# Kernel optimization log

Measured on AMD Instinct MI355X. Metric: run time of the kernel, lower is better.

## Reference

```python
import jax, jax.numpy as jnp
import numpy as np

C = 512
GROUPS = 8
EPS = 1e-5


def setup_inputs() -> dict:
    key = jax.random.key(0)
    ks = jax.random.split(key, 7)
    B, H, W = 16, 32, 32
    x = jax.random.normal(ks[0], (B, C, H, W), dtype=jnp.float32)
    gamma = jnp.ones((C,), jnp.float32)
    beta = jnp.zeros((C,), jnp.float32)
    # 1x1 convs stored as [out, in] matrices
    w_qkv = jax.random.normal(ks[1], (3 * C, C), dtype=jnp.float32) * (1.0 / np.sqrt(C))
    b_qkv = jax.random.normal(ks[2], (3 * C,), dtype=jnp.float32) * 0.02
    w_proj = jax.random.normal(ks[3], (C, C), dtype=jnp.float32) * (1.0 / np.sqrt(C))
    b_proj = jax.random.normal(ks[4], (C,), dtype=jnp.float32) * 0.02
    return {"x": x, "gamma": gamma, "beta": beta, "w_qkv": w_qkv,
            "b_qkv": b_qkv, "w_proj": w_proj, "b_proj": b_proj}


def _group_norm(x, gamma, beta):
    B, Cc, H, W = x.shape
    xg = x.reshape(B, GROUPS, Cc // GROUPS, H, W)
    mean = xg.mean(axis=(2, 3, 4), keepdims=True)
    var = xg.var(axis=(2, 3, 4), keepdims=True)
    xg = (xg - mean) * jax.lax.rsqrt(var + EPS)
    x = xg.reshape(B, Cc, H, W)
    return x * gamma[None, :, None, None] + beta[None, :, None, None]


def reference(x, gamma, beta, w_qkv, b_qkv, w_proj, b_proj):
    B, Cc, H, W = x.shape
    N = H * W
    h = _group_norm(x, gamma, beta)  # [B,C,H,W]
    hf = h.reshape(B, Cc, N)  # [B,C,N]
    # 1x1 conv == matmul over channel dim
    qkv = jnp.einsum('oc,bcn->bon', w_qkv, hf) + b_qkv[None, :, None]  # [B,3C,N]
    q, k, v = jnp.split(qkv, 3, axis=1)  # each [B,C,N]
    scale = 1.0 / jnp.sqrt(jnp.float32(Cc))
    # attn[b,i,j] = sum_c q[b,c,i] * k[b,c,j]
    attn = jnp.einsum('bci,bcj->bij', q, k) * scale  # [B,N,N]
    attn = jax.nn.softmax(attn, axis=-1)
    out = jnp.einsum('bij,bcj->bci', attn, v)  # [B,C,N]
    out = jnp.einsum('oc,bcn->bon', w_proj, out) + b_proj[None, :, None]
    return x + out.reshape(B, Cc, H, W)
```

## Files before the change

kernel.cpp:

```cpp
#include <hip/hip_runtime.h>
#include <hip/hip_bf16.h>

typedef unsigned short u16;
typedef unsigned int u32;
typedef __attribute__((ext_vector_type(8))) short short8;
typedef __attribute__((ext_vector_type(4))) float floatx4;

#define BATCH 16
#define CDIM 512
#define NSPAT 1024
#define NGROUP 8

__device__ __forceinline__ u16 f2bf(float f) {
    unsigned u = __float_as_uint(f);
    u += 0x7FFFu + ((u >> 16) & 1u);
    return (u16)(u >> 16);
}
__device__ __forceinline__ u32 f2bf2(float lo, float hi) {
    __hip_bfloat162 h = __float22bfloat162_rn(make_float2(lo, hi));
    return *(u32*)&h;
}

__device__ __forceinline__ void load_lds16(const void* g, void* l) {
    __builtin_amdgcn_global_load_lds(
        (const __attribute__((address_space(1))) unsigned int*)g,
        (__attribute__((address_space(3))) unsigned int*)l, 16, 0, 0);
}

__global__ __launch_bounds__(256) void prep_kernel(
    const float* __restrict__ w_qkv, const float* __restrict__ w_proj,
    const float* __restrict__ b_qkv, const float* __restrict__ x,
    u16* __restrict__ wmega, u16* __restrict__ wproj_bf, u16* __restrict__ wv_t,
    float* __restrict__ stats, float* __restrict__ lsums, float* __restrict__ bpv) {
    int b = blockIdx.x;
    int tid = threadIdx.x;
    if (b < 768) {
        const float* src = (b < 512) ? w_qkv : w_proj;
        u16* dst = (b < 512) ? wmega : wproj_bf;
        int i = (b < 512 ? b : b - 512) * 256 + tid;
        float4 v = ((const float4*)src)[i];
        u32* d = (u32*)dst;
        d[i * 2] = f2bf2(v.x, v.y);
        d[i * 2 + 1] = f2bf2(v.z, v.w);
        return;
    }
    if (b < 832) {
        __shared__ u16 t[64 * 66];
        int bt = b - 768;
        int tx = bt & 7, ty = bt >> 3;
        const float* src = w_qkv + (size_t)(1024 + ty * 64) * CDIM + tx * 64;
#pragma unroll
        for (int p = 0; p < 4; ++p) {
            int r = p * 16 + (tid >> 4);
            int c4 = (tid & 15) << 2;
            float4 v = *(const float4*)(src + (size_t)r * CDIM + c4);
            u16* d = &t[r * 66 + c4];
            d[0] = f2bf(v.x); d[1] = f2bf(v.y); d[2] = f2bf(v.z); d[3] = f2bf(v.w);
        }
        __syncthreads();
        u16* dst = wv_t + (size_t)(tx * 64) * CDIM + ty * 64;
#pragma unroll
        for (int p = 0; p < 4; ++p) {
            int c = p * 16 + (tid >> 4);
            int r4 = (tid & 15) << 2;
            ushort4 o;
            o.x = t[(r4 + 0) * 66 + c];
            o.y = t[(r4 + 1) * 66 + c];
            o.z = t[(r4 + 2) * 66 + c];
            o.w = t[(r4 + 3) * 66 + c];
            *(ushort4*)(dst + (size_t)c * CDIM + r4) = o;
        }
        return;
    }
    if (b < 960) {
        __shared__ float rs[4], rss[4];
        int bg = b - 832;
        const float4* xv = (const float4*)(x + (size_t)bg * 65536);
        float s = 0.f, ss = 0.f;
        for (int i = tid; i < 16384; i += 256) {
            float4 v = xv[i];
            s += v.x + v.y + v.z + v.w;
            ss += v.x * v.x + v.y * v.y + v.z * v.z + v.w * v.w;
        }
#pragma unroll
        for (int off = 32; off; off >>= 1) { s += __shfl_down(s, off); ss += __shfl_down(ss, off); }
        int wave = tid >> 6, lane = tid & 63;
        if (lane == 0) { rs[wave] = s; rss[wave] = ss; }
        __syncthreads();
        if (tid == 0) {
            float S1 = rs[0] + rs[1] + rs[2] + rs[3];
            float S2 = rss[0] + rss[1] + rss[2] + rss[3];
            float mean = S1 * (1.f / 65536.f);
            float var = S2 * (1.f / 65536.f) - mean * mean;
            stats[bg * 2] = mean;
            stats[bg * 2 + 1] = rsqrtf(var + 1e-5f);
        }
        return;
    }
    if (b < 976) {
        ((float4*)lsums)[(b - 960) * 256 + tid] = (float4){0.f, 0.f, 0.f, 0.f};
        return;
    }
    {
        int o0 = (b - 976) * 64;
        int wave = tid >> 6, lane = tid & 63;
        const float4* bvv = (const float4*)(b_qkv + 1024);
        float4 v0 = bvv[lane * 2], v1 = bvv[lane * 2 + 1];
        for (int it = 0; it < 16; ++it) {
            int o = o0 + wave * 16 + it;
            const float4* wr = (const float4*)(w_proj + (size_t)o * CDIM);
            float4 a0 = wr[lane * 2], a1 = wr[lane * 2 + 1];
            float s = a0.x * v0.x + a0.y * v0.y + a0.z * v0.z + a0.w * v0.w
                    + a1.x * v1.x + a1.y * v1.y + a1.z * v1.z + a1.w * v1.w;
#pragma unroll
            for (int off = 32; off; off >>= 1) s += __shfl_down(s, off);
            if (lane == 0) bpv[o] = s;
        }
    }
}

__device__ __forceinline__ void gemm_core(
    const u16* __restrict__ Ab, const u16* __restrict__ Bb, int K, int lda, int ldb,
    int m0, int n0, u16* As, u16* Bs, floatx4 (&acc)[4][4]) {
    int tid = threadIdx.x;
    int lane = tid & 63, wave = tid >> 6, quad = lane >> 4, lrow = lane & 15;
    int wm = (wave >> 1) << 6, wn = (wave & 1) << 6;
    for (int k0 = 0; k0 < K; k0 += 64) {
#pragma unroll
        for (int it = 0; it < 4; ++it) {
            int c = it * 256 + tid;
            int r = c >> 3, p = c & 7;
            int kc = p ^ (r & 7);
            load_lds16(Ab + (size_t)(m0 + r) * lda + k0 + (kc << 3), &As[c << 3]);
            load_lds16(Bb + (size_t)(n0 + r) * ldb + k0 + (kc << 3), &Bs[c << 3]);
        }
        __syncthreads();
#pragma unroll
        for (int s = 0; s < 2; ++s) {
            short8 af[4], bf[4];
#pragma unroll
            for (int i = 0; i < 4; ++i) {
                int R = wm + i * 16 + lrow;
                int p = (s * 4 + quad) ^ (R & 7);
                af[i] = *(const short8*)&As[(R << 6) + (p << 3)];
            }
#pragma unroll
            for (int j = 0; j < 4; ++j) {
                int R = wn + j * 16 + lrow;
                int p = (s * 4 + quad) ^ (R & 7);
                bf[j] = *(const short8*)&Bs[(R << 6) + (p << 3)];
            }
#pragma unroll
            for (int i = 0; i < 4; ++i)
#pragma unroll
                for (int j = 0; j < 4; ++j)
                    acc[i][j] = __builtin_amdgcn_mfma_f32_16x16x32_bf16(af[i], bf[j], acc[i][j], 0, 0, 0);
        }
        __syncthreads();
    }
}

#define ACC_INIT floatx4 acc[4][4]; \
    _Pragma("unroll") for (int i = 0; i < 4; ++i) \
    _Pragma("unroll") for (int j = 0; j < 4; ++j) acc[i][j] = (floatx4){0.f, 0.f, 0.f, 0.f};

#define EPILOG_IDX int lane = threadIdx.x & 63, wave = threadIdx.x >> 6; \
    int quad = lane >> 4, lrow = lane & 15; \
    int wm = (wave >> 1) << 6, wn = (wave & 1) << 6;

#define TSTR 66
__global__ __launch_bounds__(256) void gn_wpv_kernel(
    const float* __restrict__ x, const float* __restrict__ gamma, const float* __restrict__ beta,
    const float* __restrict__ stats, u16* __restrict__ hT,
    const u16* __restrict__ wproj_bf, const u16* __restrict__ wv_t, u16* __restrict__ wmega) {
    __shared__ u16 smem[2 * 128 * 64];
    int tid = threadIdx.x;
    if (blockIdx.z == 16) {
        if (blockIdx.x >= 4 || blockIdx.y >= 4) return;
        int m0 = blockIdx.y << 7, n0 = blockIdx.x << 7;
        ACC_INIT;
        gemm_core(wproj_bf, wv_t, CDIM, CDIM, CDIM, m0, n0, smem, smem + 128 * 64, acc);
        EPILOG_IDX;
#pragma unroll
        for (int i = 0; i < 4; ++i)
#pragma unroll
            for (int j = 0; j < 4; ++j)
#pragma unroll
                for (int r = 0; r < 4; ++r) {
                    int R = m0 + wm + i * 16 + (quad << 2) + r;
                    int Cc = n0 + wn + j * 16 + lrow;
                    wmega[(size_t)(1024 + R) * CDIM + Cc] = f2bf(acc[i][j][r]);
                }
        return;
    }
    u16* t = smem;
    int b = blockIdx.z, c0 = blockIdx.y << 6, n0 = blockIdx.x << 6;
    const float* xb = x + ((size_t)b * CDIM + c0) * NSPAT + n0;
#pragma unroll
    for (int p = 0; p < 4; ++p) {
        int cl = p * 16 + (tid >> 4);
        int nl = (tid & 15) << 2;
        int c = c0 + cl;
        int bg = b * NGROUP + (c >> 6);
        float ga = gamma[c] * stats[bg * 2 + 1];
        float be = beta[c] - stats[bg * 2] * ga;
        float4 v = *(const float4*)(xb + (size_t)cl * NSPAT + nl);
        u16* dst = &t[cl * TSTR + nl];
        dst[0] = f2bf(v.x * ga + be);
        dst[1] = f2bf(v.y * ga + be);
        dst[2] = f2bf(v.z * ga + be);
        dst[3] = f2bf(v.w * ga + be);
    }
    __syncthreads();
    u16* hb = hT + ((size_t)b * NSPAT + n0) * CDIM + c0;
#pragma unroll
    for (int p = 0; p < 4; ++p) {
        int nl = p * 16 + (tid >> 4);
        int cl4 = (tid & 15) << 2;
        ushort4 o;
        o.x = t[(cl4 + 0) * TSTR + nl];
        o.y = t[(cl4 + 1) * TSTR + nl];
        o.z = t[(cl4 + 2) * TSTR + nl];
        o.w = t[(cl4 + 3) * TSTR + nl];
        *(ushort4*)(hb + (size_t)nl * CDIM + cl4) = o;
    }
}

__global__ __launch_bounds__(256) void qkv_kernel(
    const u16* __restrict__ wmega, const u16* __restrict__ hT,
    const float* __restrict__ b_qkv, const float* __restrict__ bpv,
    u16* __restrict__ qkT, u16* __restrict__ WV) {
    __shared__ u16 As[128 * 64];
    __shared__ u16 Bs[128 * 64];
    int z = blockIdx.x;
    int n0 = blockIdx.y << 7;
    int m0 = blockIdx.z << 7;
    const u16* Bb = hT + (size_t)z * CDIM * NSPAT;
    ACC_INIT;
    gemm_core(wmega, Bb, CDIM, CDIM, CDIM, m0, n0, As, Bs, acc);
    EPILOG_IDX;
    if (blockIdx.z < 8) {
        u16* qk = qkT + (size_t)z * NSPAT * NSPAT;
#pragma unroll
        for (int i = 0; i < 4; ++i)
#pragma unroll
            for (int j = 0; j < 4; ++j) {
                int R0 = m0 + wm + i * 16 + (quad << 2);
                int Cc = n0 + wn + j * 16 + lrow;
                uint2 u;
                u.x = f2bf2(acc[i][j][0] + b_qkv[R0 + 0], acc[i][j][1] + b_qkv[R0 + 1]);
                u.y = f2bf2(acc[i][j][2] + b_qkv[R0 + 2], acc[i][j][3] + b_qkv[R0 + 3]);
                *(uint2*)&qk[(size_t)Cc * NSPAT + R0] = u;
            }
    } else {
        u16* Wp = WV + (size_t)z * CDIM * NSPAT;
#pragma unroll
        for (int i = 0; i < 4; ++i)
#pragma unroll
            for (int j = 0; j < 4; ++j)
#pragma unroll
                for (int r = 0; r < 4; ++r) {
                    int R = m0 - 1024 + wm + i * 16 + (quad << 2) + r;
                    int Cc = n0 + wn + j * 16 + lrow;
                    Wp[(size_t)R * NSPAT + Cc] = f2bf(acc[i][j][r] + bpv[R]);
                }
    }
}

__global__ __launch_bounds__(256) void scores_kernel(
    const u16* __restrict__ qkT, u16* __restrict__ P, float* __restrict__ lsums, float scale) {
    __shared__ u16 As[128 * 64];
    __shared__ u16 Bs[128 * 64];
    int z = blockIdx.x;
    int n0 = blockIdx.y << 7;
    int m0 = blockIdx.z << 7;
    const u16* qb = qkT + (size_t)z * NSPAT * NSPAT;
    ACC_INIT;
    gemm_core(qb + CDIM, qb, CDIM, NSPAT, NSPAT, m0, n0, As, Bs, acc);
    EPILOG_IDX;
    u16* Pp = P + (size_t)z * NSPAT * NSPAT;
    float* ls = lsums + (size_t)z * NSPAT;
#pragma unroll
    for (int nj = 0; nj < 4; ++nj) {
        int Ci = n0 + wn + nj * 16 + lrow;
        float part = 0.f;
#pragma unroll
        for (int mi = 0; mi < 4; ++mi) {
            int Rj0 = m0 + wm + mi * 16 + (quad << 2);
            float e0 = __expf(acc[mi][nj][0] * scale);
            float e1 = __expf(acc[mi][nj][1] * scale);
            float e2 = __expf(acc[mi][nj][2] * scale);
            float e3 = __expf(acc[mi][nj][3] * scale);
            part += (e0 + e1) + (e2 + e3);
            uint2 u;
            u.x = f2bf2(e0, e1);
            u.y = f2bf2(e2, e3);
            *(uint2*)&Pp[(size_t)Ci * NSPAT + Rj0] = u;
        }
        part += __shfl_xor(part, 16);
        part += __shfl_xor(part, 32);
        if (lane < 16) atomicAdd(&ls[Ci], part);
    }
}

__global__ __launch_bounds__(256) void final_kernel(
    const u16* __restrict__ WV, const u16* __restrict__ P, const float* __restrict__ lsums,
    const float* __restrict__ bias, const float* __restrict__ x, float* __restrict__ out) {
    __shared__ u16 As[128 * 64];
    __shared__ u16 Bs[128 * 64];
    int z = blockIdx.x;
    int n0 = blockIdx.y << 7;
    int m0 = blockIdx.z << 7;
    const u16* Pb = P + (size_t)z * NSPAT * NSPAT;
    const u16* WVb = WV + (size_t)z * CDIM * NSPAT;
    ACC_INIT;
    gemm_core(Pb, WVb, NSPAT, NSPAT, NSPAT, m0, n0, As, Bs, acc);
    EPILOG_IDX;
    float* Op = out + (size_t)z * CDIM * NSPAT;
    const float* xr = x + (size_t)z * CDIM * NSPAT;
    const float* li = lsums + (size_t)z * NSPAT;
#pragma unroll
    for (int mi = 0; mi < 4; ++mi) {
        int Ri0 = m0 + wm + mi * 16 + (quad << 2);
        float4 lv = *(const float4*)&li[Ri0];
        float s0 = __builtin_amdgcn_rcpf(lv.x);
        float s1 = __builtin_amdgcn_rcpf(lv.y);
        float s2 = __builtin_amdgcn_rcpf(lv.z);
        float s3 = __builtin_amdgcn_rcpf(lv.w);
#pragma unroll
        for (int nj = 0; nj < 4; ++nj) {
            int Co = n0 + wn + nj * 16 + lrow;
            float bv = bias[Co];
            size_t off = (size_t)Co * NSPAT + Ri0;
            float4 xv = *(const float4*)&xr[off];
            float4 o;
            o.x = acc[mi][nj][0] * s0 + bv + xv.x;
            o.y = acc[mi][nj][1] * s1 + bv + xv.y;
            o.z = acc[mi][nj][2] * s2 + bv + xv.z;
            o.w = acc[mi][nj][3] * s3 + bv + xv.w;
            *(float4*)&Op[off] = o;
        }
    }
}

extern "C" void kernel_launch(void* const* d_in, const int* in_sizes, int n_in,
                              void* d_out, int out_size, void* d_ws, size_t ws_size,
                              hipStream_t stream) {
    const float* x      = (const float*)d_in[0];
    const float* gamma  = (const float*)d_in[1];
    const float* beta   = (const float*)d_in[2];
    const float* w_qkv  = (const float*)d_in[3];
    const float* b_qkv  = (const float*)d_in[4];
    const float* w_proj = (const float*)d_in[5];
    const float* b_proj = (const float*)d_in[6];
    float* out = (float*)d_out;

    const size_t CN = (size_t)CDIM * NSPAT;
    const size_t NN = (size_t)NSPAT * NSPAT;
    const float SCALE = 0.044194173824159216f;

    char* ws = (char*)d_ws;
    float* stats   = (float*)ws;
    float* bpv     = (float*)(ws + 1024);
    u16* wmega     = (u16*)(ws + 4096);
    u16* wproj_bf  = wmega + (size_t)3 * CDIM * CDIM;
    u16* wv_t      = wproj_bf + (size_t)CDIM * CDIM;
    u16* hT        = wv_t + (size_t)CDIM * CDIM;
    u16* qkT       = hT + BATCH * CN;
    u16* WV        = qkT + BATCH * NN;
    u16* P         = WV + BATCH * CN;
    float* lsums   = (float*)(P + BATCH * NN);

    prep_kernel<<<984, 256, 0, stream>>>(
        w_qkv, w_proj, b_qkv, x, wmega, wproj_bf, wv_t, stats, lsums, bpv);

    gn_wpv_kernel<<<dim3(16, 8, 17), 256, 0, stream>>>(
        x, gamma, beta, stats, hT, wproj_bf, wv_t, wmega);

    qkv_kernel<<<dim3(BATCH, 8, 12), 256, 0, stream>>>(
        wmega, hT, b_qkv, bpv, qkT, WV);

    scores_kernel<<<dim3(BATCH, 8, 8), 256, 0, stream>>>(qkT, P, lsums, SCALE);

    final_kernel<<<dim3(BATCH, 4, 8), 256, 0, stream>>>(WV, P, lsums, b_proj, x, out);
}
```

Before: 148.0 us.

## Double-buffer LDS tiles in GEMM core to overlap global loads with MFMA

Adds a double-buffered variant of the shared GEMM core: the next K tile is staged into a second LDS buffer via global_load_lds while MFMAs run on the current tile. A partial vmcnt wait and scheduling barriers replace the full sync, hiding global-memory latency in the qkv, scores and final GEMM kernels. This doubles LDS per block to 64KB, which may reduce occupancy, and relies on the hand-tuned vmcnt count matching the number of outstanding loads.

New measurement: 142.8 us. 3.5% less time.

```diff
diff --git a/kernel.cpp b/kernel.cpp
--- a/kernel.cpp
+++ b/kernel.cpp
@@ -119,44 +119,80 @@
     }
 }
 
+__device__ __forceinline__ void stage_tile(
+    const u16* __restrict__ Ab, const u16* __restrict__ Bb, int lda, int ldb,
+    int m0, int n0, int k0, u16* As, u16* Bs) {
+    int tid = threadIdx.x;
+#pragma unroll
+    for (int it = 0; it < 4; ++it) {
+        int c = it * 256 + tid;
+        int r = c >> 3, p = c & 7;
+        int kc = p ^ (r & 7);
+        load_lds16(Ab + (size_t)(m0 + r) * lda + k0 + (kc << 3), &As[c << 3]);
+        load_lds16(Bb + (size_t)(n0 + r) * ldb + k0 + (kc << 3), &Bs[c << 3]);
+    }
+}
+
+__device__ __forceinline__ void compute_tile(
+    const u16* As, const u16* Bs, int wm, int wn, int quad, int lrow,
+    floatx4 (&acc)[4][4]) {
+#pragma unroll
+    for (int s = 0; s < 2; ++s) {
+        short8 af[4], bf[4];
+#pragma unroll
+        for (int i = 0; i < 4; ++i) {
+            int R = wm + i * 16 + lrow;
+            int p = (s * 4 + quad) ^ (R & 7);
+            af[i] = *(const short8*)&As[(R << 6) + (p << 3)];
+        }
+#pragma unroll
+        for (int j = 0; j < 4; ++j) {
+            int R = wn + j * 16 + lrow;
+            int p = (s * 4 + quad) ^ (R & 7);
+            bf[j] = *(const short8*)&Bs[(R << 6) + (p << 3)];
+        }
+#pragma unroll
+        for (int i = 0; i < 4; ++i)
+#pragma unroll
+            for (int j = 0; j < 4; ++j)
+                acc[i][j] = __builtin_amdgcn_mfma_f32_16x16x32_bf16(af[i], bf[j], acc[i][j], 0, 0, 0);
+    }
+}
+
+template <bool DB>
 __device__ __forceinline__ void gemm_core(
     const u16* __restrict__ Ab, const u16* __restrict__ Bb, int K, int lda, int ldb,
     int m0, int n0, u16* As, u16* Bs, floatx4 (&acc)[4][4]) {
     int tid = threadIdx.x;
     int lane = tid & 63, wave = tid >> 6, quad = lane >> 4, lrow = lane & 15;
     int wm = (wave >> 1) << 6, wn = (wave & 1) << 6;
-    for (int k0 = 0; k0 < K; k0 += 64) {
-#pragma unroll
-        for (int it = 0; it < 4; ++it) {
-            int c = it * 256 + tid;
-            int r = c >> 3, p = c & 7;
-            int kc = p ^ (r & 7);
-            load_lds16(Ab + (size_t)(m0 + r) * lda + k0 + (kc << 3), &As[c << 3]);
-            load_lds16(Bb + (size_t)(n0 + r) * ldb + k0 + (kc << 3), &Bs[c << 3]);
-        }
-        __syncthreads();
-#pragma unroll
-        for (int s = 0; s < 2; ++s) {
-            short8 af[4], bf[4];
-#pragma unroll
-            for (int i = 0; i < 4; ++i) {
-                int R = wm + i * 16 + lrow;
-                int p = (s * 4 + quad) ^ (R & 7);
-                af[i] = *(const short8*)&As[(R << 6) + (p << 3)];
-            }
-#pragma unroll
-            for (int j = 0; j < 4; ++j) {
-                int R = wn + j * 16 + lrow;
-                int p = (s * 4 + quad) ^ (R & 7);
-                bf[j] = *(const short8*)&Bs[(R << 6) + (p << 3)];
-            }
-#pragma unroll
-            for (int i = 0; i < 4; ++i)
-#pragma unroll
-                for (int j = 0; j < 4; ++j)
-                    acc[i][j] = __builtin_amdgcn_mfma_f32_16x16x32_bf16(af[i], bf[j], acc[i][j], 0, 0, 0);
-        }
-        __syncthreads();
+    if constexpr (!DB) {
+        for (int k0 = 0; k0 < K; k0 += 64) {
+            stage_tile(Ab, Bb, lda, ldb, m0, n0, k0, As, Bs);
+            __syncthreads();
+            compute_tile(As, Bs, wm, wn, quad, lrow, acc);
+            __syncthreads();
+        }
+    } else {
+        const int TS = 128 * 64;
+        int nt = K >> 6;
+        stage_tile(Ab, Bb, lda, ldb, m0, n0, 0, As, Bs);
+        u16 *Ac = As, *Bc = Bs, *An = As + TS, *Bn = Bs + TS;
+        for (int t = 0; t < nt - 1; ++t) {
+            stage_tile(Ab, Bb, lda, ldb, m0, n0, (t + 1) << 6, An, Bn);
+            asm volatile("s_waitcnt vmcnt(8)" ::: "memory");
+            __builtin_amdgcn_s_barrier();
+            __builtin_amdgcn_sched_barrier(0);
+            compute_tile(Ac, Bc, wm, wn, quad, lrow, acc);
+            __builtin_amdgcn_sched_barrier(0);
+            __builtin_amdgcn_s_barrier();
+            u16* t0 = Ac; Ac = An; An = t0;
+            u16* t1 = Bc; Bc = Bn; Bn = t1;
+        }
+        asm volatile("s_waitcnt vmcnt(0)" ::: "memory");
+        __builtin_amdgcn_s_barrier();
+        __builtin_amdgcn_sched_barrier(0);
+        compute_tile(Ac, Bc, wm, wn, quad, lrow, acc);
     }
 }
 
@@ -179,7 +215,7 @@
         if (blockIdx.x >= 4 || blockIdx.y >= 4) return;
         int m0 = blockIdx.y << 7, n0 = blockIdx.x << 7;
         ACC_INIT;
-        gemm_core(wproj_bf, wv_t, CDIM, CDIM, CDIM, m0, n0, smem, smem + 128 * 64, acc);
+        gemm_core<false>(wproj_bf, wv_t, CDIM, CDIM, CDIM, m0, n0, smem, smem + 128 * 64, acc);
         EPILOG_IDX;
 #pragma unroll
         for (int i = 0; i < 4; ++i)
@@ -230,14 +266,14 @@
     const u16* __restrict__ wmega, const u16* __restrict__ hT,
     const float* __restrict__ b_qkv, const float* __restrict__ bpv,
     u16* __restrict__ qkT, u16* __restrict__ WV) {
-    __shared__ u16 As[128 * 64];
-    __shared__ u16 Bs[128 * 64];
+    __shared__ u16 As[2 * 128 * 64];
+    __shared__ u16 Bs[2 * 128 * 64];
     int z = blockIdx.x;
     int n0 = blockIdx.y << 7;
     int m0 = blockIdx.z << 7;
     const u16* Bb = hT + (size_t)z * CDIM * NSPAT;
     ACC_INIT;
-    gemm_core(wmega, Bb, CDIM, CDIM, CDIM, m0, n0, As, Bs, acc);
+    gemm_core<true>(wmega, Bb, CDIM, CDIM, CDIM, m0, n0, As, Bs, acc);
     EPILOG_IDX;
     if (blockIdx.z < 8) {
         u16* qk = qkT + (size_t)z * NSPAT * NSPAT;
@@ -269,14 +305,14 @@
 
 __global__ __launch_bounds__(256) void scores_kernel(
     const u16* __restrict__ qkT, u16* __restrict__ P, float* __restrict__ lsums, float scale) {
-    __shared__ u16 As[128 * 64];
-    __shared__ u16 Bs[128 * 64];
+    __shared__ u16 As[2 * 128 * 64];
+    __shared__ u16 Bs[2 * 128 * 64];
     int z = blockIdx.x;
     int n0 = blockIdx.y << 7;
     int m0 = blockIdx.z << 7;
     const u16* qb = qkT + (size_t)z * NSPAT * NSPAT;
     ACC_INIT;
-    gemm_core(qb + CDIM, qb, CDIM, NSPAT, NSPAT, m0, n0, As, Bs, acc);
+    gemm_core<true>(qb + CDIM, qb, CDIM, NSPAT, NSPAT, m0, n0, As, Bs, acc);
     EPILOG_IDX;
     u16* Pp = P + (size_t)z * NSPAT * NSPAT;
     float* ls = lsums + (size_t)z * NSPAT;
@@ -306,15 +342,15 @@
 __global__ __launch_bounds__(256) void final_kernel(
     const u16* __restrict__ WV, const u16* __restrict__ P, const float* __restrict__ lsums,
     const float* __restrict__ bias, const float* __restrict__ x, float* __restrict__ out) {
-    __shared__ u16 As[128 * 64];
-    __shared__ u16 Bs[128 * 64];
+    __shared__ u16 As[2 * 128 * 64];
+    __shared__ u16 Bs[2 * 128 * 64];
     int z = blockIdx.x;
     int n0 = blockIdx.y << 7;
     int m0 = blockIdx.z << 7;
     const u16* Pb = P + (size_t)z * NSPAT * NSPAT;
     const u16* WVb = WV + (size_t)z * CDIM * NSPAT;
     ACC_INIT;
-    gemm_core(Pb, WVb, NSPAT, NSPAT, NSPAT, m0, n0, As, Bs, acc);
+    gemm_core<true>(Pb, WVb, NSPAT, NSPAT, NSPAT, m0, n0, As, Bs, acc);
     EPILOG_IDX;
     float* Op = out + (size_t)z * CDIM * NSPAT;
     const float* xr = x + (size_t)z * CDIM * NSPAT;
```

## Use 256x128 double-buffered 8-wave GEMM with phased prefetch in main kernels

Applied to the files above, without the earlier changes.

Replaces the 128x128 single-buffered 4-wave GEMM core in the qkv, scores and final kernels with a 256x128 tile computed by 512 threads. The K loop double-buffers LDS and issues the next tiles' global-to-LDS loads in four interleaved phases, with explicit vmcnt waits, barriers and raised MFMA priority. The goal is to hide global load latency behind MFMA work and raise data reuse per block. The cost is 96KB of dynamic LDS per block, fewer blocks per launch, and fragile hand-written waitcnt and barrier scheduling.

Result: no change. 149.9 us (+1.2%).

```diff
diff --git a/kernel.cpp b/kernel.cpp
--- a/kernel.cpp
+++ b/kernel.cpp
@@ -119,43 +119,56 @@
     }
 }
 
-__device__ __forceinline__ void gemm_core(
+__device__ __forceinline__ void stage_tile(
+    const u16* __restrict__ Ab, const u16* __restrict__ Bb, int lda, int ldb,
+    int m0, int n0, int k0, u16* As, u16* Bs) {
+    int tid = threadIdx.x;
+#pragma unroll
+    for (int it = 0; it < 4; ++it) {
+        int c = it * 256 + tid;
+        int r = c >> 3, p = c & 7;
+        int kc = p ^ (r & 7);
+        load_lds16(Ab + (size_t)(m0 + r) * lda + k0 + (kc << 3), &As[c << 3]);
+        load_lds16(Bb + (size_t)(n0 + r) * ldb + k0 + (kc << 3), &Bs[c << 3]);
+    }
+}
+
+__device__ __forceinline__ void compute_tile(
+    const u16* As, const u16* Bs, int wm, int wn, int quad, int lrow,
+    floatx4 (&acc)[4][4]) {
+#pragma unroll
+    for (int s = 0; s < 2; ++s) {
+        short8 af[4], bf[4];
+#pragma unroll
+        for (int i = 0; i < 4; ++i) {
+            int R = wm + i * 16 + lrow;
+            int p = (s * 4 + quad) ^ (R & 7);
+            af[i] = *(const short8*)&As[(R << 6) + (p << 3)];
+        }
+#pragma unroll
+        for (int j = 0; j < 4; ++j) {
+            int R = wn + j * 16 + lrow;
+            int p = (s * 4 + quad) ^ (R & 7);
+            bf[j] = *(const short8*)&Bs[(R << 6) + (p << 3)];
+        }
+#pragma unroll
+        for (int i = 0; i < 4; ++i)
+#pragma unroll
+            for (int j = 0; j < 4; ++j)
+                acc[i][j] = __builtin_amdgcn_mfma_f32_16x16x32_bf16(af[i], bf[j], acc[i][j], 0, 0, 0);
+    }
+}
+
+__device__ __forceinline__ void gemm_core_sb(
     const u16* __restrict__ Ab, const u16* __restrict__ Bb, int K, int lda, int ldb,
     int m0, int n0, u16* As, u16* Bs, floatx4 (&acc)[4][4]) {
     int tid = threadIdx.x;
     int lane = tid & 63, wave = tid >> 6, quad = lane >> 4, lrow = lane & 15;
     int wm = (wave >> 1) << 6, wn = (wave & 1) << 6;
     for (int k0 = 0; k0 < K; k0 += 64) {
-#pragma unroll
-        for (int it = 0; it < 4; ++it) {
-            int c = it * 256 + tid;
-            int r = c >> 3, p = c & 7;
-            int kc = p ^ (r & 7);
-            load_lds16(Ab + (size_t)(m0 + r) * lda + k0 + (kc << 3), &As[c << 3]);
-            load_lds16(Bb + (size_t)(n0 + r) * ldb + k0 + (kc << 3), &Bs[c << 3]);
-        }
+        stage_tile(Ab, Bb, lda, ldb, m0, n0, k0, As, Bs);
         __syncthreads();
-#pragma unroll
-        for (int s = 0; s < 2; ++s) {
-            short8 af[4], bf[4];
-#pragma unroll
-            for (int i = 0; i < 4; ++i) {
-                int R = wm + i * 16 + lrow;
-                int p = (s * 4 + quad) ^ (R & 7);
-                af[i] = *(const short8*)&As[(R << 6) + (p << 3)];
-            }
-#pragma unroll
-            for (int j = 0; j < 4; ++j) {
-                int R = wn + j * 16 + lrow;
-                int p = (s * 4 + quad) ^ (R & 7);
-                bf[j] = *(const short8*)&Bs[(R << 6) + (p << 3)];
-            }
-#pragma unroll
-            for (int i = 0; i < 4; ++i)
-#pragma unroll
-                for (int j = 0; j < 4; ++j)
-                    acc[i][j] = __builtin_amdgcn_mfma_f32_16x16x32_bf16(af[i], bf[j], acc[i][j], 0, 0, 0);
-        }
+        compute_tile(As, Bs, wm, wn, quad, lrow, acc);
         __syncthreads();
     }
 }
@@ -167,6 +180,108 @@
 #define EPILOG_IDX int lane = threadIdx.x & 63, wave = threadIdx.x >> 6; \
     int quad = lane >> 4, lrow = lane & 15; \
     int wm = (wave >> 1) << 6, wn = (wave & 1) << 6;
+
+#define TSA 16384
+#define TSB 8192
+
+__device__ __forceinline__ void issueA(
+    const u16* __restrict__ Ab, int lda, int m0, int t, int h, u16* smem) {
+    int tid = threadIdx.x;
+    u16* base = smem + (t & 1) * TSA + h * 8192;
+#pragma unroll
+    for (int l = 0; l < 2; ++l) {
+        int c = l * 512 + tid;
+        int ridx = c >> 3, p = c & 7;
+        int kc = p ^ (ridx & 7);
+        int r = ((ridx >> 6) << 7) + (h << 6) + (ridx & 63);
+        load_lds16(Ab + (size_t)(m0 + r) * lda + (t << 6) + (kc << 3), base + (c << 3));
+    }
+}
+
+__device__ __forceinline__ void issueB(
+    const u16* __restrict__ Bb, int ldb, int n0, int t, int h, u16* smem) {
+    int tid = threadIdx.x;
+    u16* base = smem + 2 * TSA + (t & 1) * TSB + h * 4096;
+    int ridx = tid >> 3, p = tid & 7;
+    int kc = p ^ (ridx & 7);
+    int r = ((ridx >> 4) << 5) + (h << 4) + (ridx & 15);
+    load_lds16(Bb + (size_t)(n0 + r) * ldb + (t << 6) + (kc << 3), base + (tid << 3));
+}
+
+__device__ __forceinline__ void comp_phase(
+    const u16* smem, int slot, int qm, int qn,
+    int wrow, int wcol, int quad, int lrow, floatx4 (&acc)[8][2]) {
+    const u16* Abase = smem + slot * TSA + qm * 8192;
+    const u16* Bbase = smem + 2 * TSA + slot * TSB + qn * 4096;
+    short8 af[8];
+    short8 bf[2];
+#pragma unroll
+    for (int ks = 0; ks < 2; ++ks) {
+#pragma unroll
+        for (int i = 0; i < 4; ++i) {
+            int ridx = wrow * 64 + i * 16 + lrow;
+            int p = (ks * 4 + quad) ^ (ridx & 7);
+            af[ks * 4 + i] = *(const short8*)&Abase[(ridx << 6) + (p << 3)];
+        }
+        int ridxb = wcol * 16 + lrow;
+        int pb = (ks * 4 + quad) ^ (ridxb & 7);
+        bf[ks] = *(const short8*)&Bbase[(ridxb << 6) + (pb << 3)];
+    }
+    asm volatile("s_waitcnt lgkmcnt(0)" ::: "memory");
+    __builtin_amdgcn_sched_barrier(0);
+    __builtin_amdgcn_s_setprio(1);
+#pragma unroll
+    for (int ks = 0; ks < 2; ++ks)
+#pragma unroll
+        for (int i = 0; i < 4; ++i)
+            acc[qm * 4 + i][qn] = __builtin_amdgcn_mfma_f32_16x16x32_bf16(
+                af[ks * 4 + i], bf[ks], acc[qm * 4 + i][qn], 0, 0, 0);
+    __builtin_amdgcn_s_setprio(0);
+}
+
+#define PHASE_BAR  __builtin_amdgcn_s_barrier(); __builtin_amdgcn_sched_barrier(0);
+
+__device__ __forceinline__ void gemm256(
+    const u16* __restrict__ Ab, const u16* __restrict__ Bb, int K, int lda, int ldb,
+    int m0, int n0, u16* smem, floatx4 (&acc)[8][2]) {
+    int tid = threadIdx.x;
+    int lane = tid & 63, wave = tid >> 6;
+    int quad = lane >> 4, lrow = lane & 15;
+    int wrow = wave >> 2, wcol = wave & 3;
+    int nt = K >> 6;
+    issueA(Ab, lda, m0, 0, 0, smem);
+    issueA(Ab, lda, m0, 0, 1, smem);
+    issueB(Bb, ldb, n0, 0, 0, smem);
+    issueB(Bb, ldb, n0, 0, 1, smem);
+    issueA(Ab, lda, m0, 1, 0, smem);
+    issueB(Bb, ldb, n0, 1, 0, smem);
+    for (int t = 0; t < nt; ++t) {
+        int slot = t & 1;
+        if (t + 1 < nt) { asm volatile("s_waitcnt vmcnt(3)" ::: "memory"); }
+        else            { asm volatile("s_waitcnt vmcnt(0)" ::: "memory"); }
+        PHASE_BAR;
+        if (t + 1 < nt) issueA(Ab, lda, m0, t + 1, 1, smem);
+        comp_phase(smem, slot, 0, 0, wrow, wcol, quad, lrow, acc);
+        PHASE_BAR;
+        if (t + 1 < nt) issueB(Bb, ldb, n0, t + 1, 1, smem);
+        comp_phase(smem, slot, 0, 1, wrow, wcol, quad, lrow, acc);
+        PHASE_BAR;
+        if (t + 2 < nt) issueA(Ab, lda, m0, t + 2, 0, smem);
+        comp_phase(smem, slot, 1, 0, wrow, wcol, quad, lrow, acc);
+        PHASE_BAR;
+        if (t + 2 < nt) issueB(Bb, ldb, n0, t + 2, 0, smem);
+        comp_phase(smem, slot, 1, 1, wrow, wcol, quad, lrow, acc);
+    }
+    __builtin_amdgcn_sched_barrier(0);
+}
+
+#define ACC_INIT8 floatx4 acc[8][2]; \
+    _Pragma("unroll") for (int i = 0; i < 8; ++i) \
+    _Pragma("unroll") for (int j = 0; j < 2; ++j) acc[i][j] = (floatx4){0.f, 0.f, 0.f, 0.f};
+
+#define EPILOG_IDX8 int lane = threadIdx.x & 63, wave = threadIdx.x >> 6; \
+    int quad = lane >> 4, lrow = lane & 15; \
+    int wrow = wave >> 2, wcol = wave & 3;
 
 #define TSTR 66
 __global__ __launch_bounds__(256) void gn_wpv_kernel(
@@ -179,7 +294,7 @@
         if (blockIdx.x >= 4 || blockIdx.y >= 4) return;
         int m0 = blockIdx.y << 7, n0 = blockIdx.x << 7;
         ACC_INIT;
-        gemm_core(wproj_bf, wv_t, CDIM, CDIM, CDIM, m0, n0, smem, smem + 128 * 64, acc);
+        gemm_core_sb(wproj_bf, wv_t, CDIM, CDIM, CDIM, m0, n0, smem, smem + 128 * 64, acc);
         EPILOG_IDX;
 #pragma unroll
         for (int i = 0; i < 4; ++i)
@@ -226,71 +341,69 @@
     }
 }
 
-__global__ __launch_bounds__(256) void qkv_kernel(
+__global__ __launch_bounds__(512, 2) void qkv_kernel(
     const u16* __restrict__ wmega, const u16* __restrict__ hT,
     const float* __restrict__ b_qkv, const float* __restrict__ bpv,
     u16* __restrict__ qkT, u16* __restrict__ WV) {
-    __shared__ u16 As[128 * 64];
-    __shared__ u16 Bs[128 * 64];
+    extern __shared__ u16 smem[];
     int z = blockIdx.x;
     int n0 = blockIdx.y << 7;
-    int m0 = blockIdx.z << 7;
+    int m0 = blockIdx.z << 8;
     const u16* Bb = hT + (size_t)z * CDIM * NSPAT;
-    ACC_INIT;
-    gemm_core(wmega, Bb, CDIM, CDIM, CDIM, m0, n0, As, Bs, acc);
-    EPILOG_IDX;
-    if (blockIdx.z < 8) {
+    ACC_INIT8;
+    gemm256(wmega, Bb, CDIM, CDIM, CDIM, m0, n0, smem, acc);
+    EPILOG_IDX8;
+    if (blockIdx.z < 4) {
         u16* qk = qkT + (size_t)z * NSPAT * NSPAT;
 #pragma unroll
-        for (int i = 0; i < 4; ++i)
-#pragma unroll
-            for (int j = 0; j < 4; ++j) {
-                int R0 = m0 + wm + i * 16 + (quad << 2);
-                int Cc = n0 + wn + j * 16 + lrow;
+        for (int mf = 0; mf < 8; ++mf)
+#pragma unroll
+            for (int nf = 0; nf < 2; ++nf) {
+                int R0 = m0 + wrow * 128 + mf * 16 + (quad << 2);
+                int Cc = n0 + wcol * 32 + nf * 16 + lrow;
                 uint2 u;
-                u.x = f2bf2(acc[i][j][0] + b_qkv[R0 + 0], acc[i][j][1] + b_qkv[R0 + 1]);
-                u.y = f2bf2(acc[i][j][2] + b_qkv[R0 + 2], acc[i][j][3] + b_qkv[R0 + 3]);
+                u.x = f2bf2(acc[mf][nf][0] + b_qkv[R0 + 0], acc[mf][nf][1] + b_qkv[R0 + 1]);
+                u.y = f2bf2(acc[mf][nf][2] + b_qkv[R0 + 2], acc[mf][nf][3] + b_qkv[R0 + 3]);
                 *(uint2*)&qk[(size_t)Cc * NSPAT + R0] = u;
             }
     } else {
         u16* Wp = WV + (size_t)z * CDIM * NSPAT;
 #pragma unroll
-        for (int i = 0; i < 4; ++i)
-#pragma unroll
-            for (int j = 0; j < 4; ++j)
+        for (int mf = 0; mf < 8; ++mf)
+#pragma unroll
+            for (int nf = 0; nf < 2; ++nf)
 #pragma unroll
                 for (int r = 0; r < 4; ++r) {
-                    int R = m0 - 1024 + wm + i * 16 + (quad << 2) + r;
-                    int Cc = n0 + wn + j * 16 + lrow;
-                    Wp[(size_t)R * NSPAT + Cc] = f2bf(acc[i][j][r] + bpv[R]);
+                    int R = m0 - 1024 + wrow * 128 + mf * 16 + (quad << 2) + r;
+                    int Cc = n0 + wcol * 32 + nf * 16 + lrow;
+                    Wp[(size_t)R * NSPAT + Cc] = f2bf(acc[mf][nf][r] + bpv[R]);
                 }
     }
 }
 
-__global__ __launch_bounds__(256) void scores_kernel(
+__global__ __launch_bounds__(512, 2) void scores_kernel(
     const u16* __restrict__ qkT, u16* __restrict__ P, float* __restrict__ lsums, float scale) {
-    __shared__ u16 As[128 * 64];
-    __shared__ u16 Bs[128 * 64];
+    extern __shared__ u16 smem[];
     int z = blockIdx.x;
     int n0 = blockIdx.y << 7;
-    int m0 = blockIdx.z << 7;
+    int m0 = blockIdx.z << 8;
     const u16* qb = qkT + (size_t)z * NSPAT * NSPAT;
-    ACC_INIT;
-    gemm_core(qb + CDIM, qb, CDIM, NSPAT, NSPAT, m0, n0, As, Bs, acc);
-    EPILOG_IDX;
+    ACC_INIT8;
+    gemm256(qb + CDIM, qb, CDIM, NSPAT, NSPAT, m0, n0, smem, acc);
+    EPILOG_IDX8;
     u16* Pp = P + (size_t)z * NSPAT * NSPAT;
     float* ls = lsums + (size_t)z * NSPAT;
 #pragma unroll
-    for (int nj = 0; nj < 4; ++nj) {
-        int Ci = n0 + wn + nj * 16 + lrow;
+    for (int nf = 0; nf < 2; ++nf) {
+        int Ci = n0 + wcol * 32 + nf * 16 + lrow;
         float part = 0.f;
 #pragma unroll
-        for (int mi = 0; mi < 4; ++mi) {
-            int Rj0 = m0 + wm + mi * 16 + (quad << 2);
-            float e0 = __expf(acc[mi][nj][0] * scale);
-            float e1 = __expf(acc[mi][nj][1] * scale);
-            float e2 = __expf(acc[mi][nj][2] * scale);
-            float e3 = __expf(acc[mi][nj][3] * scale);
+        for (int mf = 0; mf < 8; ++mf) {
+            int Rj0 = m0 + wrow * 128 + mf * 16 + (quad << 2);
+            float e0 = __expf(acc[mf][nf][0] * scale);
+            float e1 = __expf(acc[mf][nf][1] * scale);
+            float e2 = __expf(acc[mf][nf][2] * scale);
+            float e3 = __expf(acc[mf][nf][3] * scale);
             part += (e0 + e1) + (e2 + e3);
             uint2 u;
             u.x = f2bf2(e0, e1);
@@ -303,41 +416,40 @@
     }
 }
 
-__global__ __launch_bounds__(256) void final_kernel(
+__global__ __launch_bounds__(512, 2) void final_kernel(
     const u16* __restrict__ WV, const u16* __restrict__ P, const float* __restrict__ lsums,
     const float* __restrict__ bias, const float* __restrict__ x, float* __restrict__ out) {
-    __shared__ u16 As[128 * 64];
-    __shared__ u16 Bs[128 * 64];
+    extern __shared__ u16 smem[];
     int z = blockIdx.x;
     int n0 = blockIdx.y << 7;
-    int m0 = blockIdx.z << 7;
+    int m0 = blockIdx.z << 8;
     const u16* Pb = P + (size_t)z * NSPAT * NSPAT;
     const u16* WVb = WV + (size_t)z * CDIM * NSPAT;
-    ACC_INIT;
-    gemm_core(Pb, WVb, NSPAT, NSPAT, NSPAT, m0, n0, As, Bs, acc);
-    EPILOG_IDX;
+    ACC_INIT8;
+    gemm256(Pb, WVb, NSPAT, NSPAT, NSPAT, m0, n0, smem, acc);
+    EPILOG_IDX8;
     float* Op = out + (size_t)z * CDIM * NSPAT;
     const float* xr = x + (size_t)z * CDIM * NSPAT;
     const float* li = lsums + (size_t)z * NSPAT;
 #pragma unroll
-    for (int mi = 0; mi < 4; ++mi) {
-        int Ri0 = m0 + wm + mi * 16 + (quad << 2);
+    for (int mf = 0; mf < 8; ++mf) {
+        int Ri0 = m0 + wrow * 128 + mf * 16 + (quad << 2);
         float4 lv = *(const float4*)&li[Ri0];
         float s0 = __builtin_amdgcn_rcpf(lv.x);
         float s1 = __builtin_amdgcn_rcpf(lv.y);
         float s2 = __builtin_amdgcn_rcpf(lv.z);
         float s3 = __builtin_amdgcn_rcpf(lv.w);
 #pragma unroll
-        for (int nj = 0; nj < 4; ++nj) {
-            int Co = n0 + wn + nj * 16 + lrow;
+        for (int nf = 0; nf < 2; ++nf) {
+            int Co = n0 + wcol * 32 + nf * 16 + lrow;
             float bv = bias[Co];
             size_t off = (size_t)Co * NSPAT + Ri0;
             float4 xv = *(const float4*)&xr[off];
             float4 o;
-            o.x = acc[mi][nj][0] * s0 + bv + xv.x;
-            o.y = acc[mi][nj][1] * s1 + bv + xv.y;
-            o.z = acc[mi][nj][2] * s2 + bv + xv.z;
-            o.w = acc[mi][nj][3] * s3 + bv + xv.w;
+            o.x = acc[mf][nf][0] * s0 + bv + xv.x;
+            o.y = acc[mf][nf][1] * s1 + bv + xv.y;
+            o.z = acc[mf][nf][2] * s2 + bv + xv.z;
+            o.w = acc[mf][nf][3] * s3 + bv + xv.w;
             *(float4*)&Op[off] = o;
         }
     }
@@ -358,6 +470,7 @@
     const size_t CN = (size_t)CDIM * NSPAT;
     const size_t NN = (size_t)NSPAT * NSPAT;
     const float SCALE = 0.044194173824159216f;
+    const int LDS_BYTES = 2 * (TSA + TSB) * 2;
 
     char* ws = (char*)d_ws;
     float* stats   = (float*)ws;
@@ -377,10 +490,10 @@
     gn_wpv_kernel<<<dim3(16, 8, 17), 256, 0, stream>>>(
         x, gamma, beta, stats, hT, wproj_bf, wv_t, wmega);
 
-    qkv_kernel<<<dim3(BATCH, 8, 12), 256, 0, stream>>>(
+    qkv_kernel<<<dim3(BATCH, 8, 6), 512, LDS_BYTES, stream>>>(
         wmega, hT, b_qkv, bpv, qkT, WV);
 
-    scores_kernel<<<dim3(BATCH, 8, 8), 256, 0, stream>>>(qkT, P, lsums, SCALE);
-
-    final_kernel<<<dim3(BATCH, 4, 8), 256, 0, stream>>>(WV, P, lsums, b_proj, x, out);
-}
+    scores_kernel<<<dim3(BATCH, 8, 4), 512, LDS_BYTES, stream>>>(qkT, P, lsums, SCALE);
+
+    final_kernel<<<dim3(BATCH, 4, 4), 512, LDS_BYTES, stream>>>(WV, P, lsums, b_proj, x, out);
+}
```
